# Kernel tuning notes

Hardware: AMD Instinct MI355X
Metric: run time of the kernel (lower is better)

The kernel has to match this reference:

```python
import jax, jax.numpy as jnp
import numpy as np

DT = 0.001      # time step (matches dt=0.001 in calculate_state)
GAMMA = 2.0     # velocity damping of the relaxation dynamics
L = 1.0         # rest edge length (Strctr.L)


def _energy(x_flat, buckle, thetas_ss, rest_lengths, k_stiff, k_soft, k_stretch):
    """Total potential energy of the 2D chain (rotation hinges + edge stretch)."""
    pos = x_flat.reshape(-1, 2)                    # (N, 2)
    v = pos[1:] - pos[:-1]                         # (E, 2) edge vectors, E = H+1
    edge_len = jnp.sqrt(jnp.sum(v * v, axis=1))    # (E,)
    v1, v2 = v[:-1], v[1:]                         # (H, 2) consecutive edges per hinge
    cross = v1[:, 0] * v2[:, 1] - v1[:, 1] * v2[:, 0]
    dot = jnp.sum(v1 * v2, axis=1)
    thetas = jnp.arctan2(cross, dot)               # (H,) signed hinge angles
    T = thetas[:, None]                            # (H, 1)
    TH = thetas_ss[:, None]                        # (H, 1)
    stiff_mask = ((buckle == 1) & (T > -TH)) | ((buckle == -1) & (T < TH))  # (H, S)
    k_rot = jnp.where(stiff_mask, k_stiff, k_soft)
    rotation_energy = 0.5 * jnp.sum(k_rot * (T - TH) ** 2)
    stretch_energy = 0.5 * jnp.sum(k_stretch * (edge_len - rest_lengths) ** 2)
    return rotation_energy + stretch_energy


def setup_inputs() -> dict:
    key = jax.random.key(0)
    H, S = 32768, 4
    N = H + 2
    k1, k2, k3 = jax.random.split(key, 3)
    # straight chain along x with tiny transverse noise (realistic init geometry)
    base = jnp.stack([jnp.arange(N, dtype=jnp.float32) * L,
                      jnp.zeros((N,), jnp.float32)], axis=1)
    init_pos = base + 0.01 * jax.random.normal(k1, (N, 2), jnp.float32)
    buckle = (2 * jax.random.randint(k2, (H, S), 0, 2) - 1).astype(jnp.int32)  # +/-1
    thetas_ss = 0.2 * jax.random.uniform(k3, (H,), jnp.float32) - 0.1
    rest_lengths = jnp.full((H + 1,), L, dtype=jnp.float32)
    return dict(init_pos=init_pos, buckle=buckle, thetas_ss=thetas_ss,
                rest_lengths=rest_lengths,
                k_stiff=jnp.float32(10.0), k_soft=jnp.float32(0.1),
                k_stretch=jnp.float32(100.0), n_steps=1000)


def reference(init_pos, buckle, thetas_ss, rest_lengths, k_stiff, k_soft, k_stretch, n_steps):
    n_coords = init_pos.size
    # first two nodes (4 DOFs) clamped, tip_loc=None branch
    fixed = jnp.zeros((n_coords,), bool).at[jnp.arange(4)].set(True)
    fixed_vals = init_pos.reshape(-1)
    force = jax.grad(lambda xf: -_energy(xf, buckle, thetas_ss, rest_lengths,
                                         k_stiff, k_soft, k_stretch))
    x0 = init_pos.reshape(-1)
    v0 = jnp.zeros_like(x0)

    def step(carry, _):
        x, v = carry
        f = jnp.where(fixed, 0.0, force(x))                 # potential force on free DOFs
        v = jnp.where(fixed, 0.0, v + DT * (f - GAMMA * v)) # damped semi-implicit Euler
        x = jnp.where(fixed, fixed_vals, x + DT * v)
        return (x, v), x

    (x_final, v_final), pos_in_t = jax.lax.scan(step, (x0, v0), None, length=n_steps)
    return x_final, pos_in_t
```

## Files before the change

### kernel.cpp

```cpp
#include <hip/hip_runtime.h>

#define DT 0.001f
#define GAMMA 2.0f

#define KSTEPS 60
#define HALOB  120
#define TILE   144
#define REGION 384
#define NW     8
#define WINT   48
#define WHALO  8
#define JEXCH  4
#define NTHREADS 512

typedef float v2f __attribute__((ext_vector_type(2)));

__device__ __forceinline__ void lds_barrier() {
    asm volatile("s_waitcnt lgkmcnt(0)" ::: "memory");
    __builtin_amdgcn_s_barrier();
    asm volatile("" ::: "memory");
}

__device__ __forceinline__ float dpp_shl1(float x) {
    return __int_as_float(__builtin_amdgcn_update_dpp(
        0, __float_as_int(x), 0x130, 0xF, 0xF, true));
}
__device__ __forceinline__ float dpp_shr1(float x) {
    return __int_as_float(__builtin_amdgcn_update_dpp(
        0, __float_as_int(x), 0x138, 0xF, 0xF, true));
}

__global__ __launch_bounds__(256) void init_state(const float* __restrict__ init_pos,
                                                  float* __restrict__ x,
                                                  float* __restrict__ v,
                                                  int n_coords) {
    int i = blockIdx.x * blockDim.x + threadIdx.x;
    if (i < n_coords) { x[i] = init_pos[i]; v[i] = 0.0f; }
}

__global__ __launch_bounds__(NTHREADS) void chunk_kernel(
    const float* __restrict__ xin, const float* __restrict__ vin,
    float* __restrict__ xout, float* __restrict__ vout,
    const int*   __restrict__ buckle,
    const float* __restrict__ thetas_ss,
    const float* __restrict__ rest_len,
    const float* __restrict__ kstiff_p,
    const float* __restrict__ ksoft_p,
    const float* __restrict__ kstretch_p,
    const float* __restrict__ init_pos,
    float* __restrict__ out,
    int N, int H, int n_coords, int t0, int ksteps, int n_steps)
{
    __shared__ float4 xch[2][REGION];

    const int lane = threadIdx.x & 63;
    const int w    = threadIdx.x >> 6;
    const int r    = w * WINT + lane - WHALO;
    const int tile_start = blockIdx.x * TILE;
    const int jg   = tile_start - HALOB + r;
    const bool rvalid = (r >= 0) && (r < REGION);
    const bool nvalid = (jg >= 0) && (jg < N);
    const int  jc   = min(max(jg, 0), N - 1);

    const float kS  = kstiff_p[0];
    const float kw  = ksoft_p[0];
    const float kst = kstretch_p[0];

    const bool edge_ok  = (jg >= 0) && (jg <= N - 2);
    const bool hinge_ok = (jg >= 0) && (jg < H);

    const float rl     = rest_len[min(max(jg, 0), H)];
    const float emask  = edge_ok ? 1.0f : 0.0f;
    const float efix   = edge_ok ? 0.0f : 1.0f;
    const float kst_l  = edge_ok ? kst : 0.0f;
    const float kstrl  = kst * rl;
    const float hfix   = hinge_ok ? 0.0f : 1.0f;
    float tss = 0.0f, npf = 0.0f;
    if (hinge_ok) {
        tss = thetas_ss[jg];
        int4 b = reinterpret_cast<const int4*>(buckle)[jg];
        npf = (float)((b.x == 1) + (b.y == 1) + (b.z == 1) + (b.w == 1));
    }
    const float ntss  = -tss;
    const float npf4m = 4.0f - npf;
    const float dKl   = hinge_ok ? (kS - kw) : 0.0f;
    const float kw4l  = hinge_ok ? 4.0f * kw : 0.0f;

    const bool pinned = nvalid && (jg < 2);
    v2f pin = {0.0f, 0.0f};
    if (pinned) { pin.x = init_pos[2 * jg]; pin.y = init_pos[2 * jg + 1]; }

    const bool wave_int = (lane >= WHALO) && (lane < WHALO + WINT);
    const bool writer   = wave_int && (r >= HALOB) && (r < HALOB + TILE) && nvalid;

    float2 P0 = reinterpret_cast<const float2*>(xin)[jc];
    float2 V0 = reinterpret_cast<const float2*>(vin)[jc];
    v2f p = {P0.x, P0.y};
    v2f v = {V0.x, V0.y};

    float2* tptr = reinterpret_cast<float2*>(out + (size_t)(t0 + 1) * (size_t)n_coords) + jc;
    const size_t tstride = (size_t)(n_coords / 2);

    const float C998 = 1.0f - GAMMA * DT;

    for (int s0 = 0; s0 < ksteps; s0 += JEXCH) {
        if (s0 > 0) {
            int buf = (s0 >> 2) & 1;
            if (wave_int && rvalid) xch[buf][r] = make_float4(p.x, p.y, v.x, v.y);
            lds_barrier();
            if (rvalid) {
                float4 f4 = xch[buf][r];
                p.x = f4.x; p.y = f4.y; v.x = f4.z; v.y = f4.w;
            }
        }
        float2 sbuf[JEXCH];
        #pragma unroll
        for (int u = 0; u < JEXCH; ++u) {
            v2f q;  q.x  = dpp_shl1(p.x); q.y  = dpp_shl1(p.y);
            v2f e  = q - p;
            v2f en; en.x = dpp_shl1(e.x); en.y = dpp_shl1(e.y);

            float l2   = fmaf(e.x, e.x, fmaf(e.y, e.y, efix));
            float irt  = __builtin_amdgcn_rsqf(l2) * emask;
            float il2  = irt * irt;
            float se   = fmaf(-kstrl, irt, kst_l);

            float cr = e.x * en.y - e.y * en.x;
            float dd = fmaf(e.x, en.x, fmaf(e.y, en.y, hfix));
            float t  = cr * __builtin_amdgcn_rcpf(dd);
            float t2 = t * t;
            float pp = -0.0040540580f;
            pp = fmaf(pp, t2,  0.0218612288f);
            pp = fmaf(pp, t2, -0.0559098861f);
            pp = fmaf(pp, t2,  0.0964200441f);
            pp = fmaf(pp, t2, -0.1390853351f);
            pp = fmaf(pp, t2,  0.1994653599f);
            pp = fmaf(pp, t2, -0.3332985605f);
            pp = fmaf(pp, t2,  0.9999993329f);
            float th   = pp * t;
            float thmt = th - tss;
            float ns = (th > ntss ? npf : 0.0f) + (th < tss ? npf4m : 0.0f);
            float K  = fmaf(ns, dKl, kw4l);
            float g  = K * thmt;

            float gm   = dpp_shr1(g);
            float coef = (gm - g) * il2;
            v2f F;
            F.x = fmaf(coef, -e.y, se * e.x);
            F.y = fmaf(coef,  e.x, se * e.y);
            v2f Fp; Fp.x = dpp_shr1(F.x); Fp.y = dpp_shr1(F.y);

            v2f f = F - Fp;
            v = v * C998 + f * DT;
            p = p + v * DT;
            if (tile_start == 0) {
                if (pinned) { v.x = 0.0f; v.y = 0.0f; p = pin; }
            }
            sbuf[u] = make_float2(p.x, p.y);
        }
        if (writer) {
            #pragma unroll
            for (int u = 0; u < JEXCH; ++u) {
                tptr[(size_t)u * tstride] = sbuf[u];
            }
        }
        tptr += (size_t)JEXCH * tstride;
    }

    if (writer) {
        reinterpret_cast<float2*>(xout)[jg] = make_float2(p.x, p.y);
        reinterpret_cast<float2*>(vout)[jg] = make_float2(v.x, v.y);
        if (t0 + ksteps == n_steps) {
            reinterpret_cast<float2*>(out)[jg] = make_float2(p.x, p.y);
        }
    }
}

extern "C" void kernel_launch(void* const* d_in, const int* in_sizes, int n_in,
                              void* d_out, int out_size, void* d_ws, size_t ws_size,
                              hipStream_t stream) {
    const float* init_pos  = (const float*)d_in[0];
    const int*   buckle    = (const int*)d_in[1];
    const float* thetas_ss = (const float*)d_in[2];
    const float* rest_len  = (const float*)d_in[3];
    const float* kstiff    = (const float*)d_in[4];
    const float* ksoft     = (const float*)d_in[5];
    const float* kstretch  = (const float*)d_in[6];

    const int n_coords = in_sizes[0];
    const int N = n_coords / 2;
    const int H = in_sizes[2];
    const int n_steps = out_size / n_coords - 1;

    float* out = (float*)d_out;
    float* wsf = (float*)d_ws;
    float* sAx = wsf;
    float* sAv = wsf + n_coords;
    float* sBx = wsf + 2 * n_coords;
    float* sBv = wsf + 3 * n_coords;

    init_state<<<(n_coords + 255) / 256, 256, 0, stream>>>(init_pos, sAx, sAv, n_coords);

    const int nblocks = (N + TILE - 1) / TILE;
    float* xin = sAx; float* vin = sAv;
    float* xout = sBx; float* vout = sBv;
    for (int t0 = 0; t0 < n_steps; t0 += KSTEPS) {
        int k = n_steps - t0; if (k > KSTEPS) k = KSTEPS;
        chunk_kernel<<<nblocks, NTHREADS, 0, stream>>>(
            xin, vin, xout, vout,
            buckle, thetas_ss, rest_len, kstiff, ksoft, kstretch,
            init_pos, out, N, H, n_coords, t0, k, n_steps);
        float* t1 = xin; xin = xout; xout = t1;
        float* t2 = vin; vin = vout; vout = t2;
    }
}
```

Before: 297.8 us.

## Fuse chunk launches into one persistent kernel with neighbor-flag synchronization

Replaces the sequence of per-chunk kernel launches, plus the init kernel, with one persistent kernel. Between phases each block publishes its state to a ping-pong global buffer and spins on its two neighbours' flags before reading halo values. This removes per-launch overhead and the grid-wide barrier implied by kernel boundaries. In exchange it relies on all blocks being co-resident (about 229 blocks of 512 threads) and adds spin-wait latency and extra memory-fence traffic.

```diff
diff --git a/kernel.cpp b/kernel.cpp
--- a/kernel.cpp
+++ b/kernel.cpp
@@ -30,33 +30,34 @@
         0, __float_as_int(x), 0x138, 0xF, 0xF, true));
 }
 
-__global__ __launch_bounds__(256) void init_state(const float* __restrict__ init_pos,
-                                                  float* __restrict__ x,
-                                                  float* __restrict__ v,
-                                                  int n_coords) {
-    int i = blockIdx.x * blockDim.x + threadIdx.x;
-    if (i < n_coords) { x[i] = init_pos[i]; v[i] = 0.0f; }
-}
-
-__global__ __launch_bounds__(NTHREADS) void chunk_kernel(
-    const float* __restrict__ xin, const float* __restrict__ vin,
-    float* __restrict__ xout, float* __restrict__ vout,
+__device__ __forceinline__ unsigned long long pack2(float a, float b) {
+    union { float f[2]; unsigned long long u; } c; c.f[0] = a; c.f[1] = b; return c.u;
+}
+__device__ __forceinline__ v2f unpack2(unsigned long long u) {
+    union { float f[2]; unsigned long long u2; } c; c.u2 = u;
+    v2f r; r.x = c.f[0]; r.y = c.f[1]; return r;
+}
+
+__global__ __launch_bounds__(NTHREADS) void sim_kernel(
+    const float* __restrict__ init_pos,
     const int*   __restrict__ buckle,
     const float* __restrict__ thetas_ss,
     const float* __restrict__ rest_len,
     const float* __restrict__ kstiff_p,
     const float* __restrict__ ksoft_p,
     const float* __restrict__ kstretch_p,
-    const float* __restrict__ init_pos,
     float* __restrict__ out,
-    int N, int H, int n_coords, int t0, int ksteps, int n_steps)
+    float4* __restrict__ stA, float4* __restrict__ stB,
+    int* __restrict__ flags,
+    int N, int H, int n_coords, int n_steps)
 {
     __shared__ float4 xch[2][REGION];
 
     const int lane = threadIdx.x & 63;
     const int w    = threadIdx.x >> 6;
     const int r    = w * WINT + lane - WHALO;
-    const int tile_start = blockIdx.x * TILE;
+    const int b    = blockIdx.x;
+    const int tile_start = b * TILE;
     const int jg   = tile_start - HALOB + r;
     const bool rvalid = (r >= 0) && (r < REGION);
     const bool nvalid = (jg >= 0) && (jg < N);
@@ -78,8 +79,8 @@
     float tss = 0.0f, npf = 0.0f;
     if (hinge_ok) {
         tss = thetas_ss[jg];
-        int4 b = reinterpret_cast<const int4*>(buckle)[jg];
-        npf = (float)((b.x == 1) + (b.y == 1) + (b.z == 1) + (b.w == 1));
+        int4 bk = reinterpret_cast<const int4*>(buckle)[jg];
+        npf = (float)((bk.x == 1) + (bk.y == 1) + (bk.z == 1) + (bk.w == 1));
     }
     const float ntss  = -tss;
     const float npf4m = 4.0f - npf;
@@ -93,85 +94,125 @@
     const bool wave_int = (lane >= WHALO) && (lane < WHALO + WINT);
     const bool writer   = wave_int && (r >= HALOB) && (r < HALOB + TILE) && nvalid;
 
-    float2 P0 = reinterpret_cast<const float2*>(xin)[jc];
-    float2 V0 = reinterpret_cast<const float2*>(vin)[jc];
+    const size_t tstride = (size_t)(n_coords / 2);
+    const float C998 = 1.0f - GAMMA * DT;
+    const int nphases = (n_steps + KSTEPS - 1) / KSTEPS;
+
+    float2 P0 = reinterpret_cast<const float2*>(init_pos)[jc];
     v2f p = {P0.x, P0.y};
-    v2f v = {V0.x, V0.y};
-
-    float2* tptr = reinterpret_cast<float2*>(out + (size_t)(t0 + 1) * (size_t)n_coords) + jc;
-    const size_t tstride = (size_t)(n_coords / 2);
-
-    const float C998 = 1.0f - GAMMA * DT;
-
-    for (int s0 = 0; s0 < ksteps; s0 += JEXCH) {
-        if (s0 > 0) {
-            int buf = (s0 >> 2) & 1;
-            if (wave_int && rvalid) xch[buf][r] = make_float4(p.x, p.y, v.x, v.y);
-            lds_barrier();
-            if (rvalid) {
-                float4 f4 = xch[buf][r];
-                p.x = f4.x; p.y = f4.y; v.x = f4.z; v.y = f4.w;
-            }
-        }
-        float2 sbuf[JEXCH];
-        #pragma unroll
-        for (int u = 0; u < JEXCH; ++u) {
-            v2f q;  q.x  = dpp_shl1(p.x); q.y  = dpp_shl1(p.y);
-            v2f e  = q - p;
-            v2f en; en.x = dpp_shl1(e.x); en.y = dpp_shl1(e.y);
-
-            float l2   = fmaf(e.x, e.x, fmaf(e.y, e.y, efix));
-            float irt  = __builtin_amdgcn_rsqf(l2) * emask;
-            float il2  = irt * irt;
-            float se   = fmaf(-kstrl, irt, kst_l);
-
-            float cr = e.x * en.y - e.y * en.x;
-            float dd = fmaf(e.x, en.x, fmaf(e.y, en.y, hfix));
-            float t  = cr * __builtin_amdgcn_rcpf(dd);
-            float t2 = t * t;
-            float pp = -0.0040540580f;
-            pp = fmaf(pp, t2,  0.0218612288f);
-            pp = fmaf(pp, t2, -0.0559098861f);
-            pp = fmaf(pp, t2,  0.0964200441f);
-            pp = fmaf(pp, t2, -0.1390853351f);
-            pp = fmaf(pp, t2,  0.1994653599f);
-            pp = fmaf(pp, t2, -0.3332985605f);
-            pp = fmaf(pp, t2,  0.9999993329f);
-            float th   = pp * t;
-            float thmt = th - tss;
-            float ns = (th > ntss ? npf : 0.0f) + (th < tss ? npf4m : 0.0f);
-            float K  = fmaf(ns, dKl, kw4l);
-            float g  = K * thmt;
-
-            float gm   = dpp_shr1(g);
-            float coef = (gm - g) * il2;
-            v2f F;
-            F.x = fmaf(coef, -e.y, se * e.x);
-            F.y = fmaf(coef,  e.x, se * e.y);
-            v2f Fp; Fp.x = dpp_shr1(F.x); Fp.y = dpp_shr1(F.y);
-
-            v2f f = F - Fp;
-            v = v * C998 + f * DT;
-            p = p + v * DT;
-            if (tile_start == 0) {
-                if (pinned) { v.x = 0.0f; v.y = 0.0f; p = pin; }
-            }
-            sbuf[u] = make_float2(p.x, p.y);
-        }
-        if (writer) {
+    v2f v = {0.0f, 0.0f};
+
+    for (int ph = 0; ph < nphases; ++ph) {
+        const int t0 = ph * KSTEPS;
+        const int ksteps = min(KSTEPS, n_steps - t0);
+
+        float2* tptr = reinterpret_cast<float2*>(out + (size_t)(t0 + 1) * (size_t)n_coords) + jc;
+
+        for (int s0 = 0; s0 < ksteps; s0 += JEXCH) {
+            if (s0 > 0) {
+                int buf = (s0 >> 2) & 1;
+                if (wave_int && rvalid) xch[buf][r] = make_float4(p.x, p.y, v.x, v.y);
+                lds_barrier();
+                if (rvalid) {
+                    float4 f4 = xch[buf][r];
+                    p.x = f4.x; p.y = f4.y; v.x = f4.z; v.y = f4.w;
+                }
+            }
+            float2 sbuf[JEXCH];
             #pragma unroll
             for (int u = 0; u < JEXCH; ++u) {
-                tptr[(size_t)u * tstride] = sbuf[u];
-            }
-        }
-        tptr += (size_t)JEXCH * tstride;
-    }
-
-    if (writer) {
-        reinterpret_cast<float2*>(xout)[jg] = make_float2(p.x, p.y);
-        reinterpret_cast<float2*>(vout)[jg] = make_float2(v.x, v.y);
+                v2f q;  q.x  = dpp_shl1(p.x); q.y  = dpp_shl1(p.y);
+                v2f e  = q - p;
+                v2f en; en.x = dpp_shl1(e.x); en.y = dpp_shl1(e.y);
+
+                float l2   = fmaf(e.x, e.x, fmaf(e.y, e.y, efix));
+                float irt  = __builtin_amdgcn_rsqf(l2) * emask;
+                float il2  = irt * irt;
+                float se   = fmaf(-kstrl, irt, kst_l);
+
+                float cr = e.x * en.y - e.y * en.x;
+                float dd = fmaf(e.x, en.x, fmaf(e.y, en.y, hfix));
+                float t  = cr * __builtin_amdgcn_rcpf(dd);
+                float t2 = t * t;
+                float pp = -0.0040540580f;
+                pp = fmaf(pp, t2,  0.0218612288f);
+                pp = fmaf(pp, t2, -0.0559098861f);
+                pp = fmaf(pp, t2,  0.0964200441f);
+                pp = fmaf(pp, t2, -0.1390853351f);
+                pp = fmaf(pp, t2,  0.1994653599f);
+                pp = fmaf(pp, t2, -0.3332985605f);
+                pp = fmaf(pp, t2,  0.9999993329f);
+                float th   = pp * t;
+                float thmt = th - tss;
+                float ns = (th > ntss ? npf : 0.0f) + (th < tss ? npf4m : 0.0f);
+                float K  = fmaf(ns, dKl, kw4l);
+                float g  = K * thmt;
+
+                float gm   = dpp_shr1(g);
+                float coef = (gm - g) * il2;
+                v2f F;
+                F.x = fmaf(coef, -e.y, se * e.x);
+                F.y = fmaf(coef,  e.x, se * e.y);
+                v2f Fp; Fp.x = dpp_shr1(F.x); Fp.y = dpp_shr1(F.y);
+
+                v2f f = F - Fp;
+                v = v * C998 + f * DT;
+                p = p + v * DT;
+                if (tile_start == 0) {
+                    if (pinned) { v.x = 0.0f; v.y = 0.0f; p = pin; }
+                }
+                sbuf[u] = make_float2(p.x, p.y);
+            }
+            if (writer) {
+                #pragma unroll
+                for (int u = 0; u < JEXCH; ++u) {
+                    tptr[(size_t)u * tstride] = sbuf[u];
+                }
+            }
+            tptr += (size_t)JEXCH * tstride;
+        }
+
         if (t0 + ksteps == n_steps) {
-            reinterpret_cast<float2*>(out)[jg] = make_float2(p.x, p.y);
+            if (writer) {
+                reinterpret_cast<float2*>(out)[jg] = make_float2(p.x, p.y);
+            }
+            break;
+        }
+
+        float4* st = (ph & 1) ? stB : stA;
+        if (writer) {
+            unsigned long long* dst = reinterpret_cast<unsigned long long*>(&st[jg]);
+            __hip_atomic_store(dst + 0, pack2(p.x, p.y),
+                               __ATOMIC_RELAXED, __HIP_MEMORY_SCOPE_AGENT);
+            __hip_atomic_store(dst + 1, pack2(v.x, v.y),
+                               __ATOMIC_RELAXED, __HIP_MEMORY_SCOPE_AGENT);
+        }
+        asm volatile("s_waitcnt vmcnt(0)" ::: "memory");
+        __syncthreads();
+        if (threadIdx.x == 0) {
+            __hip_atomic_store(&flags[b], ph + 1,
+                               __ATOMIC_RELEASE, __HIP_MEMORY_SCOPE_AGENT);
+            if (b > 0) {
+                while (__hip_atomic_load(&flags[b - 1], __ATOMIC_ACQUIRE,
+                                         __HIP_MEMORY_SCOPE_AGENT) < ph + 1)
+                    __builtin_amdgcn_s_sleep(2);
+            }
+        }
+        if (threadIdx.x == 64 && b + 1 < (int)gridDim.x) {
+            while (__hip_atomic_load(&flags[b + 1], __ATOMIC_ACQUIRE,
+                                     __HIP_MEMORY_SCOPE_AGENT) < ph + 1)
+                __builtin_amdgcn_s_sleep(2);
+        }
+        __syncthreads();
+
+        if (!writer) {
+            const unsigned long long* src = reinterpret_cast<const unsigned long long*>(&st[jc]);
+            unsigned long long up = __hip_atomic_load(src + 0, __ATOMIC_RELAXED,
+                                                      __HIP_MEMORY_SCOPE_AGENT);
+            unsigned long long uv = __hip_atomic_load(src + 1, __ATOMIC_RELAXED,
+                                                      __HIP_MEMORY_SCOPE_AGENT);
+            p = unpack2(up);
+            v = unpack2(uv);
         }
     }
 }
@@ -193,24 +234,15 @@
     const int n_steps = out_size / n_coords - 1;
 
     float* out = (float*)d_out;
-    float* wsf = (float*)d_ws;
-    float* sAx = wsf;
-    float* sAv = wsf + n_coords;
-    float* sBx = wsf + 2 * n_coords;
-    float* sBv = wsf + 3 * n_coords;
-
-    init_state<<<(n_coords + 255) / 256, 256, 0, stream>>>(init_pos, sAx, sAv, n_coords);
+    float4* stA = (float4*)d_ws;
+    float4* stB = stA + N;
+    int* flags  = (int*)(stB + N);
 
     const int nblocks = (N + TILE - 1) / TILE;
-    float* xin = sAx; float* vin = sAv;
-    float* xout = sBx; float* vout = sBv;
-    for (int t0 = 0; t0 < n_steps; t0 += KSTEPS) {
-        int k = n_steps - t0; if (k > KSTEPS) k = KSTEPS;
-        chunk_kernel<<<nblocks, NTHREADS, 0, stream>>>(
-            xin, vin, xout, vout,
-            buckle, thetas_ss, rest_len, kstiff, ksoft, kstretch,
-            init_pos, out, N, H, n_coords, t0, k, n_steps);
-        float* t1 = xin; xin = xout; xout = t1;
-        float* t2 = vin; vin = vout; vout = t2;
-    }
-}
+
+    (void)hipMemsetAsync(flags, 0, nblocks * sizeof(int), stream);
+
+    sim_kernel<<<nblocks, NTHREADS, 0, stream>>>(
+        init_pos, buckle, thetas_ss, rest_len, kstiff, ksoft, kstretch,
+        out, stA, stB, flags, N, H, n_coords, n_steps);
+}
```

New measurement: 393.7 us. +32.2%, slower.
